# Performance work log

Measured on AMD Instinct MI355X. Metric: run time of the kernel, lower is better.

The kernel has to match this reference:

```python
import jax, jax.numpy as jnp
import numpy as np

B, T, C = 1, 2048, 1024
H = 16
D = C // H
FF = 4 * C


def layernorm(x, g, b, eps=1e-5):
    mu = jnp.mean(x, axis=-1, keepdims=True)
    var = jnp.var(x, axis=-1, keepdims=True)
    return (x - mu) * jax.lax.rsqrt(var + eps) * g + b


def setup_inputs() -> dict:
    key = jax.random.key(0)
    ks = jax.random.split(key, 16)
    s = 0.02
    return {
        "x": jax.random.normal(ks[0], (B, T, C), jnp.float32),
        "qkv_w": jax.random.normal(ks[1], (C, 3 * C), jnp.float32) * s,
        "qkv_b": jnp.zeros((3 * C,), jnp.float32),
        "out_w": jax.random.normal(ks[2], (C, C), jnp.float32) * s,
        "out_b": jnp.zeros((C,), jnp.float32),
        "ln1_g": jnp.ones((C,), jnp.float32),
        "ln1_b": jnp.zeros((C,), jnp.float32),
        "ln2_g": jnp.ones((C,), jnp.float32),
        "ln2_b": jnp.zeros((C,), jnp.float32),
        "w1": jax.random.normal(ks[3], (C, FF), jnp.float32) * s,
        "b1": jnp.zeros((FF,), jnp.float32),
        "w2": jax.random.normal(ks[4], (FF, C), jnp.float32) * s,
        "b2": jnp.zeros((C,), jnp.float32),
    }


def linear_attention(h, qkv_w, qkv_b, out_w, out_b):
    qkv = h @ qkv_w + qkv_b                      # (B,T,3C)
    q, k, v = jnp.split(qkv, 3, axis=-1)
    # (B,T,C) -> (B,H,T,D)
    reshape = lambda a: a.reshape(B, T, H, D).transpose(0, 2, 1, 3)
    q, k, v = reshape(q), reshape(k), reshape(v)
    Q = jax.nn.elu(q) + 1.0
    K = jax.nn.elu(k) + 1.0
    # causal linear attention via cumulative outer-products
    KV = jnp.einsum('bhtd,bhte->bhtde', K, v)    # (B,H,T,D,D)
    KV_cum = jnp.cumsum(KV, axis=2)
    K_cum = jnp.cumsum(K, axis=2)
    num = jnp.einsum('bhtd,bhtde->bhte', Q, KV_cum)
    den = jnp.einsum('bhtd,bhtd->bht', Q, K_cum)[..., None]
    o = num / (den + 1e-6)                       # (B,H,T,D)
    o = o.transpose(0, 2, 1, 3).reshape(B, T, C)
    return o @ out_w + out_b


def reference(x, qkv_w, qkv_b, out_w, out_b, ln1_g, ln1_b, ln2_g, ln2_b, w1, b1, w2, b2):
    x = x + linear_attention(layernorm(x, ln1_g, ln1_b), qkv_w, qkv_b, out_w, out_b)
    h = layernorm(x, ln2_g, ln2_b)
    mlp = jax.nn.gelu(h @ w1 + b1, approximate=False) @ w2 + b2
    return x + mlp
```

## Files before the change

kernel.cpp:

```cpp
#include <hip/hip_runtime.h>

typedef unsigned short u16;
typedef __bf16 bf16x8 __attribute__((ext_vector_type(8)));
typedef float f32x4 __attribute__((ext_vector_type(4)));
typedef unsigned short u16x8 __attribute__((ext_vector_type(8)));
typedef unsigned short u16x4 __attribute__((ext_vector_type(4)));

__device__ __forceinline__ float bf2f(u16 u){
  union { unsigned i; float f; } v; v.i = ((unsigned)u) << 16; return v.f;
}
__device__ __forceinline__ u16 f2bf(float f){
  union { float f; unsigned i; } v; v.f = f;
  unsigned r = v.i + 0x7FFFu + ((v.i >> 16) & 1u);
  return (u16)(r >> 16);
}
__device__ __forceinline__ float elup(float x){ return x > 0.f ? x + 1.f : expf(x); }

__device__ __forceinline__ void gload_lds16(const void* gsrc, void* ldst){
  __builtin_amdgcn_global_load_lds(
      (__attribute__((address_space(1))) void*)(unsigned long long)gsrc,
      (__attribute__((address_space(3))) void*)(unsigned)(unsigned long long)ldst,
      16, 0, 0);
}

struct TD { const float* in; u16* out; int R, Cc, cx, ntiles; };

__global__ __launch_bounds__(256) void prep(TD d0, TD d1, TD d2, TD d3,
                                            const float* __restrict__ x, const float* __restrict__ g,
                                            const float* __restrict__ b, u16* __restrict__ y){
  __shared__ u16 tile[32][33];
  __shared__ float ls[4], ls2[4];
  int bidx = blockIdx.x, tid = threadIdx.x;
  if (bidx >= 12288){
    int row = bidx - 12288;
    size_t base = (size_t)row*1024 + tid*4;
    f32x4 xv = *(const f32x4*)(x + base);
    float v0=xv[0], v1=xv[1], v2=xv[2], v3=xv[3];
    float s  = v0+v1+v2+v3;
    float s2 = v0*v0+v1*v1+v2*v2+v3*v3;
    #pragma unroll
    for (int off=32; off>0; off>>=1){ s += __shfl_xor(s, off); s2 += __shfl_xor(s2, off); }
    if ((tid & 63) == 0){ ls[tid>>6] = s; ls2[tid>>6] = s2; }
    __syncthreads();
    float ts = ls[0]+ls[1]+ls[2]+ls[3];
    float ts2 = ls2[0]+ls2[1]+ls2[2]+ls2[3];
    float mean = ts*(1.f/1024.f);
    float var  = ts2*(1.f/1024.f) - mean*mean;
    float rstd = rsqrtf(var + 1e-5f);
    f32x4 gv = *(const f32x4*)(g + tid*4);
    f32x4 bv = *(const f32x4*)(b + tid*4);
    u16x4 ov;
    ov[0]=f2bf((v0-mean)*rstd*gv[0]+bv[0]);
    ov[1]=f2bf((v1-mean)*rstd*gv[1]+bv[1]);
    ov[2]=f2bf((v2-mean)*rstd*gv[2]+bv[2]);
    ov[3]=f2bf((v3-mean)*rstd*gv[3]+bv[3]);
    *(u16x4*)(y + base) = ov;
    return;
  }
  int bb = bidx;
  TD d;
  if (bb < d0.ntiles) d = d0;
  else { bb -= d0.ntiles;
    if (bb < d1.ntiles) d = d1;
    else { bb -= d1.ntiles;
      if (bb < d2.ntiles) d = d2;
      else { bb -= d2.ntiles; d = d3; } } }
  int c0 = (bb % d.cx) * 32, r0 = (bb / d.cx) * 32;
  int tx = tid & 31, ty = tid >> 5;
  #pragma unroll
  for (int i=0;i<4;i++)
    tile[ty + i*8][tx] = f2bf(d.in[(size_t)(r0 + ty + i*8)*d.Cc + c0 + tx]);
  __syncthreads();
  #pragma unroll
  for (int i=0;i<4;i++)
    d.out[(size_t)(c0 + ty + i*8)*d.R + r0 + tx] = tile[tx][ty + i*8];
}

__global__ __launch_bounds__(256) void ln2_fused(const u16* __restrict__ P0, const u16* __restrict__ P1,
                                                 const u16* __restrict__ P2, const u16* __restrict__ P3,
                                                 const float* __restrict__ bias, const float* __restrict__ xres,
                                                 const float* __restrict__ g, const float* __restrict__ b,
                                                 float* __restrict__ x2, u16* __restrict__ h2){
  int row = blockIdx.x, tid = threadIdx.x;
  size_t base = (size_t)row*1024 + tid*4;
  u16x4 a0 = *(const u16x4*)(P0 + base);
  u16x4 a1 = *(const u16x4*)(P1 + base);
  u16x4 a2 = *(const u16x4*)(P2 + base);
  u16x4 a3 = *(const u16x4*)(P3 + base);
  f32x4 rv = *(const f32x4*)(xres + base);
  f32x4 bv = *(const f32x4*)(bias + tid*4);
  f32x4 v;
  #pragma unroll
  for (int j=0;j<4;j++) v[j] = (bf2f(a0[j])+bf2f(a1[j])) + (bf2f(a2[j])+bf2f(a3[j])) + bv[j] + rv[j];
  *(f32x4*)(x2 + base) = v;
  float s  = v[0]+v[1]+v[2]+v[3];
  float s2 = v[0]*v[0]+v[1]*v[1]+v[2]*v[2]+v[3]*v[3];
  #pragma unroll
  for (int off=32; off>0; off>>=1){ s += __shfl_xor(s, off); s2 += __shfl_xor(s2, off); }
  __shared__ float ls[4], ls2[4];
  if ((tid & 63) == 0){ ls[tid>>6] = s; ls2[tid>>6] = s2; }
  __syncthreads();
  float ts = ls[0]+ls[1]+ls[2]+ls[3];
  float ts2 = ls2[0]+ls2[1]+ls2[2]+ls2[3];
  float mean = ts*(1.f/1024.f);
  float var  = ts2*(1.f/1024.f) - mean*mean;
  float rstd = rsqrtf(var + 1e-5f);
  f32x4 gv = *(const f32x4*)(g + tid*4);
  f32x4 bb = *(const f32x4*)(b + tid*4);
  u16x4 ov;
  #pragma unroll
  for (int j=0;j<4;j++) ov[j] = f2bf((v[j]-mean)*rstd*gv[j]+bb[j]);
  *(u16x4*)(h2 + base) = ov;
}

template<int EPI>
__global__ __launch_bounds__(512, 4) void gemm_bt(const u16* __restrict__ A, const u16* __restrict__ BT,
                                                  const float* __restrict__ bias, const float* __restrict__ res,
                                                  void* __restrict__ out, int N, int K, size_t pstride){
  __shared__ u16 As[2][128*64];
  __shared__ u16 Bs[2][128*64];
  int tid = threadIdx.x;
  int w = tid >> 6, lane = tid & 63;

  unsigned flat = blockIdx.x + gridDim.x*(blockIdx.y + gridDim.y*blockIdx.z);
  unsigned nwg  = gridDim.x*gridDim.y*gridDim.z;
  unsigned logical = (flat & 7)*(nwg >> 3) + (flat >> 3);
  unsigned bx = logical % gridDim.x;
  unsigned rem = logical / gridDim.x;
  unsigned by = rem % gridDim.y;
  unsigned bz = rem / gridDim.y;

  int m0 = bx * 128, n0 = by * 128;
  int Kc = K / gridDim.z;
  int kbase = bz * Kc;
  int nt = Kc / 64;

  f32x4 acc[2][4] = {};

  int l3 = lane >> 3, l7 = lane & 7;
  const u16* aSrc = A  + (size_t)(m0 + w*16 + l3)*K + kbase + (l7 ^ l3)*8;
  const u16* bSrc = BT + (size_t)(n0 + w*16 + l3)*K + kbase + (l7 ^ l3)*8;
  int r0 = (w>>1)*32, c0 = (w&1)*64;
  int lrow = lane & 15, g4 = lane >> 4;
  int swz = (lrow & 7) << 4;

  {
    u16* aD = As[0] + w*16*64;
    u16* bD = Bs[0] + w*16*64;
    gload_lds16(aSrc,                aD);
    gload_lds16(aSrc + (size_t)8*K,  aD + 8*64);
    gload_lds16(bSrc,                bD);
    gload_lds16(bSrc + (size_t)8*K,  bD + 8*64);
  }
  __syncthreads();

  int cur = 0;
  for (int t = 0; t < nt; ++t){
    if (t + 1 < nt){
      int k0 = (t+1)*64;
      u16* aD = As[cur^1] + w*16*64;
      u16* bD = Bs[cur^1] + w*16*64;
      gload_lds16(aSrc + k0,               aD);
      gload_lds16(aSrc + (size_t)8*K + k0, aD + 8*64);
      gload_lds16(bSrc + k0,               bD);
      gload_lds16(bSrc + (size_t)8*K + k0, bD + 8*64);
    }
    const char* Ab = (const char*)As[cur];
    const char* Bb = (const char*)Bs[cur];
    #pragma unroll
    for (int kk=0; kk<2; kk++){
      int ko = (kk*64 + g4*16) ^ swz;
      bf16x8 af[2], bfv[4];
      #pragma unroll
      for (int mi=0;mi<2;mi++) af[mi]  = *(const bf16x8*)(Ab + (r0 + mi*16 + lrow)*128 + ko);
      #pragma unroll
      for (int ni=0;ni<4;ni++) bfv[ni] = *(const bf16x8*)(Bb + (c0 + ni*16 + lrow)*128 + ko);
      #pragma unroll
      for (int mi=0;mi<2;mi++)
        #pragma unroll
        for (int ni=0;ni<4;ni++)
          acc[mi][ni] = __builtin_amdgcn_mfma_f32_16x16x32_bf16(af[mi], bfv[ni], acc[mi][ni], 0, 0, 0);
    }
    __syncthreads();
    cur ^= 1;
  }

  int lgr = lane >> 4;
  u16* pout = (EPI == 3) ? ((u16*)out + (size_t)bz * pstride) : (u16*)out;
  #pragma unroll
  for (int mi=0;mi<2;mi++){
    #pragma unroll
    for (int j=0;j<4;j++){
      int row = m0 + r0 + mi*16 + lgr*4 + j;
      #pragma unroll
      for (int ni=0;ni<4;ni++){
        int col = n0 + c0 + ni*16 + lrow;
        size_t idx = (size_t)row*N + col;
        if constexpr (EPI == 3){
          pout[idx] = f2bf(acc[mi][ni][j]);
        } else {
          float v = acc[mi][ni][j] + bias[col];
          if constexpr (EPI == 0){
            ((u16*)out)[idx] = f2bf(v);
          } else {
            v = 0.5f * v * (1.f + erff(v * 0.70710678118654752f));
            ((u16*)out)[idx] = f2bf(v);
          }
        }
      }
    }
  }
}

__global__ __launch_bounds__(256) void reduce4(const u16* __restrict__ P0, const u16* __restrict__ P1,
                                               const u16* __restrict__ P2, const u16* __restrict__ P3,
                                               const float* __restrict__ bias, const float* __restrict__ res,
                                               float* __restrict__ out){
  size_t i = ((size_t)blockIdx.x*256 + threadIdx.x)*4;
  u16x4 a = *(const u16x4*)(P0 + i);
  u16x4 b = *(const u16x4*)(P1 + i);
  u16x4 c = *(const u16x4*)(P2 + i);
  u16x4 d = *(const u16x4*)(P3 + i);
  f32x4 rv = *(const f32x4*)(res + i);
  f32x4 bv = *(const f32x4*)(bias + (i & 1023));
  f32x4 o;
  #pragma unroll
  for (int j=0;j<4;j++) o[j] = (bf2f(a[j]) + bf2f(b[j])) + (bf2f(c[j]) + bf2f(d[j])) + bv[j] + rv[j];
  *(f32x4*)(out + i) = o;
}

__global__ __launch_bounds__(256) void attn_chunksum(const u16* __restrict__ qkv, float* __restrict__ S,
                                                     float* __restrict__ Ks){
  __shared__ u16 KT[64*72];
  __shared__ u16 VT[64*72];
  int c = blockIdx.x, h = blockIdx.y, tid = threadIdx.x;
  int t = tid >> 2, seg = tid & 3, e0 = seg*16;
  size_t rowb = (size_t)(c*64 + t)*3072 + h*64 + e0;
  u16x8 k0 = *(const u16x8*)(qkv + rowb + 1024);
  u16x8 k1 = *(const u16x8*)(qkv + rowb + 1032);
  u16x8 v0 = *(const u16x8*)(qkv + rowb + 2048);
  u16x8 v1 = *(const u16x8*)(qkv + rowb + 2056);
  #pragma unroll
  for (int i=0;i<8;i++){
    KT[(e0 + i)*72 + t]     = f2bf(elup(bf2f(k0[i])));
    KT[(e0 + 8 + i)*72 + t] = f2bf(elup(bf2f(k1[i])));
    VT[(e0 + i)*72 + t]     = v0[i];
    VT[(e0 + 8 + i)*72 + t] = v1[i];
  }
  __syncthreads();

  int w = tid >> 6, lane = tid & 63;
  int lr = lane & 15, lk = (lane>>4)*8, g = lane >> 4, cl = lane & 15;
  bf16x8 av_[2];
  #pragma unroll
  for (int kk=0;kk<2;kk++) av_[kk] = *(const bf16x8*)(VT + (w*16 + lr)*72 + kk*32 + lk);
  f32x4 acc[4] = {};
  #pragma unroll
  for (int di=0;di<4;di++){
    #pragma unroll
    for (int kk=0;kk<2;kk++){
      bf16x8 bk = *(const bf16x8*)(KT + (di*16 + lr)*72 + kk*32 + lk);
      acc[di] = __builtin_amdgcn_mfma_f32_16x16x32_bf16(av_[kk], bk, acc[di], 0, 0, 0);
    }
  }
  size_t base = (size_t)(h*32 + c)*4096;
  #pragma unroll
  for (int di=0;di<4;di++)
    #pragma unroll
    for (int j=0;j<4;j++)
      S[base + (size_t)(w*16 + g*4 + j)*64 + di*16 + cl] = acc[di][j];

  float s = 0.f;
  #pragma unroll
  for (int i=0;i<16;i++) s += bf2f(KT[t*72 + e0 + i]);
  s += __shfl_xor(s, 1); s += __shfl_xor(s, 2);
  if (seg == 0) Ks[(size_t)(h*32 + c)*64 + t] = s;
}

__global__ __launch_bounds__(256) void attn_prefix(float* __restrict__ S, float* __restrict__ Ks){
  int g = blockIdx.x, h = blockIdx.y, tid = threadIdx.x;
  size_t hb = (size_t)h * 32 * 4096;
  int idx = g*256 + tid;
  float run = 0.f;
  for (int c=0; c<32; c++){
    size_t p = hb + (size_t)c*4096 + idx;
    float v = S[p]; S[p] = run; run += v;
  }
  if (g == 0 && tid < 64){
    float r2 = 0.f;
    for (int c=0; c<32; c++){
      size_t p = (size_t)(h*32 + c)*64 + tid;
      float v = Ks[p]; Ks[p] = r2; r2 += v;
    }
  }
}

__global__ __launch_bounds__(256) void attn_out(const u16* __restrict__ qkv, const float* __restrict__ S,
                                                const float* __restrict__ Ks, u16* __restrict__ o){
  __shared__ u16 Qs [64*72];
  __shared__ u16 Ksh[64*72];
  __shared__ u16 VT [64*72];
  __shared__ u16 SpT[64*72];
  __shared__ u16 Am [64*72];
  __shared__ float kp[64], den[64];
  int c = blockIdx.x, h = blockIdx.y, tid = threadIdx.x;
  int t = tid >> 2, seg = tid & 3, e0 = seg*16;

  size_t rowb = (size_t)(c*64 + t)*3072 + h*64 + e0;
  u16x8 q0 = *(const u16x8*)(qkv + rowb);
  u16x8 q1 = *(const u16x8*)(qkv + rowb + 8);
  u16x8 k0 = *(const u16x8*)(qkv + rowb + 1024);
  u16x8 k1 = *(const u16x8*)(qkv + rowb + 1032);
  u16x8 v0 = *(const u16x8*)(qkv + rowb + 2048);
  u16x8 v1 = *(const u16x8*)(qkv + rowb + 2056);
  #pragma unroll
  for (int i=0;i<8;i++){
    Qs [t*72 + e0 + i]     = f2bf(elup(bf2f(q0[i])));
    Qs [t*72 + e0 + 8 + i] = f2bf(elup(bf2f(q1[i])));
    Ksh[t*72 + e0 + i]     = f2bf(elup(bf2f(k0[i])));
    Ksh[t*72 + e0 + 8 + i] = f2bf(elup(bf2f(k1[i])));
    VT [(e0 + i)*72 + t]     = v0[i];
    VT [(e0 + 8 + i)*72 + t] = v1[i];
  }
  size_t sbase = (size_t)(h*32 + c)*4096;
  {
    const f32x4* sp = (const f32x4*)(S + sbase + (size_t)t*64 + e0);
    #pragma unroll
    for (int qd=0;qd<4;qd++){
      f32x4 v = sp[qd];
      #pragma unroll
      for (int j=0;j<4;j++) SpT[t*72 + e0 + qd*4 + j] = f2bf(v[j]);
    }
  }
  if (tid < 64) kp[tid] = Ks[(size_t)(h*32 + c)*64 + tid];
  __syncthreads();

  int w = tid >> 6, lane = tid & 63;
  int lr = lane & 15, lk = (lane>>4)*8, g = lane >> 4, cl = lane & 15;

  bf16x8 aq[2];
  #pragma unroll
  for (int kk=0;kk<2;kk++) aq[kk] = *(const bf16x8*)(Qs + (w*16 + lr)*72 + kk*32 + lk);

  f32x4 acc[4] = {};
  #pragma unroll
  for (int ni=0;ni<4;ni++){
    #pragma unroll
    for (int kk=0;kk<2;kk++){
      bf16x8 bs = *(const bf16x8*)(SpT + (ni*16 + lr)*72 + kk*32 + lk);
      acc[ni] = __builtin_amdgcn_mfma_f32_16x16x32_bf16(aq[kk], bs, acc[ni], 0, 0, 0);
    }
  }
  #pragma unroll
  for (int si=0;si<4;si++){
    f32x4 qk = {};
    #pragma unroll
    for (int kk=0;kk<2;kk++){
      bf16x8 bk = *(const bf16x8*)(Ksh + (si*16 + lr)*72 + kk*32 + lk);
      qk = __builtin_amdgcn_mfma_f32_16x16x32_bf16(aq[kk], bk, qk, 0, 0, 0);
    }
    #pragma unroll
    for (int j=0;j<4;j++){
      int rowt = w*16 + g*4 + j;
      int scol = si*16 + cl;
      Am[rowt*72 + scol] = f2bf((scol <= rowt) ? qk[j] : 0.f);
    }
  }
  __syncthreads();

  {
    float dsum = 0.f;
    #pragma unroll
    for (int i=0;i<16;i++) dsum += bf2f(Am[t*72 + e0 + i]);
    #pragma unroll
    for (int i=0;i<16;i++) dsum += bf2f(Qs[t*72 + e0 + i]) * kp[e0 + i];
    dsum += __shfl_xor(dsum, 1); dsum += __shfl_xor(dsum, 2);
    if (seg == 0) den[t] = dsum;
  }
  {
    bf16x8 aa[2];
    #pragma unroll
    for (int kk=0;kk<2;kk++) aa[kk] = *(const bf16x8*)(Am + (w*16 + lr)*72 + kk*32 + lk);
    #pragma unroll
    for (int ni=0;ni<4;ni++){
      #pragma unroll
      for (int kk=0;kk<2;kk++){
        bf16x8 bv = *(const bf16x8*)(VT + (ni*16 + lr)*72 + kk*32 + lk);
        acc[ni] = __builtin_amdgcn_mfma_f32_16x16x32_bf16(aa[kk], bv, acc[ni], 0, 0, 0);
      }
    }
  }
  __syncthreads();

  #pragma unroll
  for (int j=0;j<4;j++){
    int rowt = w*16 + g*4 + j;
    float inv = 1.f/(den[rowt] + 1e-6f);
    #pragma unroll
    for (int ni=0;ni<4;ni++)
      o[(size_t)(c*64 + rowt)*1024 + h*64 + ni*16 + cl] = f2bf(acc[ni][j]*inv);
  }
}

extern "C" void kernel_launch(void* const* d_in, const int* in_sizes, int n_in,
                              void* d_out, int out_size, void* d_ws, size_t ws_size,
                              hipStream_t stream) {
  (void)in_sizes; (void)n_in; (void)out_size; (void)ws_size;
  const float* x     = (const float*)d_in[0];
  const float* qkv_w = (const float*)d_in[1];
  const float* qkv_b = (const float*)d_in[2];
  const float* out_w = (const float*)d_in[3];
  const float* out_b = (const float*)d_in[4];
  const float* ln1_g = (const float*)d_in[5];
  const float* ln1_b = (const float*)d_in[6];
  const float* ln2_g = (const float*)d_in[7];
  const float* ln2_b = (const float*)d_in[8];
  const float* w1    = (const float*)d_in[9];
  const float* b1    = (const float*)d_in[10];
  const float* w2    = (const float*)d_in[11];
  const float* b2    = (const float*)d_in[12];

  char* ws = (char*)d_ws;
  u16*   wT_qkv = (u16*)  (ws);
  u16*   wT_out = (u16*)  (ws +  6291456);
  u16*   wT_w1  = (u16*)  (ws +  8388608);
  u16*   wT_w2  = (u16*)  (ws + 16777216);
  u16*   h1     = (u16*)  (ws + 25165824);
  u16*   qkv    = (u16*)  (ws + 29360128);
  float* Ssum   = (float*)(ws + 41943040);
  float* ksum   = (float*)(ws + 50331648);
  float* x2     = (float*)(ws + 50462720);
  u16*   h2     = (u16*)  (ws + 58851328);
  u16*   o      = h1;
  u16*   a1     = qkv;
  u16*   Pa0    = (u16*)(ws + 29360128);
  size_t PaStride = 2097152;
  u16*   Pm0    = (u16*)(ws);
  u16*   Pm1    = (u16*)(ws +  4194304);
  u16*   Pm2    = (u16*)(ws +  8388608);
  u16*   Pm3    = (u16*)(ws + 12582912);
  size_t PmStride = 2097152;
  float* outp   = (float*)d_out;

  TD t0{qkv_w, wT_qkv, 1024, 3072,  96, 3072};
  TD t1{out_w, wT_out, 1024, 1024,  32, 1024};
  TD t2{w1,    wT_w1,  1024, 4096, 128, 4096};
  TD t3{w2,    wT_w2,  4096, 1024,  32, 4096};
  prep<<<14336, 256, 0, stream>>>(t0, t1, t2, t3, x, ln1_g, ln1_b, h1);

  gemm_bt<0><<<dim3(16, 24, 1), 512, 0, stream>>>(h1, wT_qkv, qkv_b, nullptr, qkv, 3072, 1024, 0);

  attn_chunksum<<<dim3(32, 16), 256, 0, stream>>>(qkv, Ssum, ksum);
  attn_prefix  <<<dim3(16, 16), 256, 0, stream>>>(Ssum, ksum);
  attn_out     <<<dim3(32, 16), 256, 0, stream>>>(qkv, Ssum, ksum, o);

  gemm_bt<3><<<dim3(16, 8, 4), 512, 0, stream>>>(o, wT_out, nullptr, nullptr, Pa0, 1024, 1024, PaStride);
  ln2_fused<<<2048, 256, 0, stream>>>(Pa0, Pa0 + PaStride, Pa0 + 2*PaStride, Pa0 + 3*PaStride,
                                      out_b, x, ln2_g, ln2_b, x2, h2);

  gemm_bt<1><<<dim3(16, 32, 1), 512, 0, stream>>>(h2, wT_w1, b1, nullptr, a1, 4096, 1024, 0);

  gemm_bt<3><<<dim3(16, 8, 4), 512, 0, stream>>>(a1, wT_w2, nullptr, nullptr, Pm0, 1024, 4096, PmStride);
  reduce4<<<2048, 256, 0, stream>>>(Pm0, Pm1, Pm2, Pm3, b2, x2, outp);
}
```

Before: 130.2 us.

## Split-K the QKV GEMM and fold partial-sum reduction into attention loads

The QKV projection now runs as a two-way split-K GEMM that writes bf16 partials. The attention chunksum and output kernels read both partials and add the bias while they load, so no separate reduction pass is needed. This is meant to put more workgroups on the GPU during the QKV GEMM. In exchange it doubles the global reads in the attention kernels and adds an extra bf16 rounding step. Separately, the weight-transpose prep kernel moves from 32x32 to 64x64 tiles so it launches fewer blocks and each thread does more work.

```diff
diff --git a/kernel.cpp b/kernel.cpp
--- a/kernel.cpp
+++ b/kernel.cpp
@@ -28,11 +28,11 @@
 __global__ __launch_bounds__(256) void prep(TD d0, TD d1, TD d2, TD d3,
                                             const float* __restrict__ x, const float* __restrict__ g,
                                             const float* __restrict__ b, u16* __restrict__ y){
-  __shared__ u16 tile[32][33];
+  __shared__ u16 tile[64][65];
   __shared__ float ls[4], ls2[4];
   int bidx = blockIdx.x, tid = threadIdx.x;
-  if (bidx >= 12288){
-    int row = bidx - 12288;
+  if (bidx >= 3072){
+    int row = bidx - 3072;
     size_t base = (size_t)row*1024 + tid*4;
     f32x4 xv = *(const f32x4*)(x + base);
     float v0=xv[0], v1=xv[1], v2=xv[2], v3=xv[3];
@@ -65,15 +65,15 @@
     else { bb -= d1.ntiles;
       if (bb < d2.ntiles) d = d2;
       else { bb -= d2.ntiles; d = d3; } } }
-  int c0 = (bb % d.cx) * 32, r0 = (bb / d.cx) * 32;
-  int tx = tid & 31, ty = tid >> 5;
-  #pragma unroll
-  for (int i=0;i<4;i++)
-    tile[ty + i*8][tx] = f2bf(d.in[(size_t)(r0 + ty + i*8)*d.Cc + c0 + tx]);
-  __syncthreads();
-  #pragma unroll
-  for (int i=0;i<4;i++)
-    d.out[(size_t)(c0 + ty + i*8)*d.R + r0 + tx] = tile[tx][ty + i*8];
+  int c0 = (bb % d.cx) * 64, r0 = (bb / d.cx) * 64;
+  int tx = tid & 63, ty = tid >> 6;
+  #pragma unroll
+  for (int i=0;i<16;i++)
+    tile[tx][ty + i*4] = f2bf(d.in[(size_t)(r0 + ty + i*4)*d.Cc + c0 + tx]);
+  __syncthreads();
+  #pragma unroll
+  for (int i=0;i<16;i++)
+    d.out[(size_t)(c0 + ty + i*4)*d.R + r0 + tx] = tile[ty + i*4][tx];
 }
 
 __global__ __launch_bounds__(256) void ln2_fused(const u16* __restrict__ P0, const u16* __restrict__ P1,
@@ -229,23 +229,29 @@
   *(f32x4*)(out + i) = o;
 }
 
-__global__ __launch_bounds__(256) void attn_chunksum(const u16* __restrict__ qkv, float* __restrict__ S,
-                                                     float* __restrict__ Ks){
+__global__ __launch_bounds__(256) void attn_chunksum(const u16* __restrict__ Q0, const u16* __restrict__ Q1,
+                                                     const float* __restrict__ qb,
+                                                     float* __restrict__ S, float* __restrict__ Ks){
   __shared__ u16 KT[64*72];
   __shared__ u16 VT[64*72];
   int c = blockIdx.x, h = blockIdx.y, tid = threadIdx.x;
   int t = tid >> 2, seg = tid & 3, e0 = seg*16;
   size_t rowb = (size_t)(c*64 + t)*3072 + h*64 + e0;
-  u16x8 k0 = *(const u16x8*)(qkv + rowb + 1024);
-  u16x8 k1 = *(const u16x8*)(qkv + rowb + 1032);
-  u16x8 v0 = *(const u16x8*)(qkv + rowb + 2048);
-  u16x8 v1 = *(const u16x8*)(qkv + rowb + 2056);
+  u16x8 k0a = *(const u16x8*)(Q0 + rowb + 1024);
+  u16x8 k1a = *(const u16x8*)(Q0 + rowb + 1032);
+  u16x8 v0a = *(const u16x8*)(Q0 + rowb + 2048);
+  u16x8 v1a = *(const u16x8*)(Q0 + rowb + 2056);
+  u16x8 k0b = *(const u16x8*)(Q1 + rowb + 1024);
+  u16x8 k1b = *(const u16x8*)(Q1 + rowb + 1032);
+  u16x8 v0b = *(const u16x8*)(Q1 + rowb + 2048);
+  u16x8 v1b = *(const u16x8*)(Q1 + rowb + 2056);
+  int cb = h*64 + e0;
   #pragma unroll
   for (int i=0;i<8;i++){
-    KT[(e0 + i)*72 + t]     = f2bf(elup(bf2f(k0[i])));
-    KT[(e0 + 8 + i)*72 + t] = f2bf(elup(bf2f(k1[i])));
-    VT[(e0 + i)*72 + t]     = v0[i];
-    VT[(e0 + 8 + i)*72 + t] = v1[i];
+    KT[(e0 + i)*72 + t]     = f2bf(elup(bf2f(k0a[i]) + bf2f(k0b[i]) + qb[1024 + cb + i]));
+    KT[(e0 + 8 + i)*72 + t] = f2bf(elup(bf2f(k1a[i]) + bf2f(k1b[i]) + qb[1024 + cb + 8 + i]));
+    VT[(e0 + i)*72 + t]     = f2bf(bf2f(v0a[i]) + bf2f(v0b[i]) + qb[2048 + cb + i]);
+    VT[(e0 + 8 + i)*72 + t] = f2bf(bf2f(v1a[i]) + bf2f(v1b[i]) + qb[2048 + cb + 8 + i]);
   }
   __syncthreads();
 
@@ -295,8 +301,10 @@
   }
 }
 
-__global__ __launch_bounds__(256) void attn_out(const u16* __restrict__ qkv, const float* __restrict__ S,
-                                                const float* __restrict__ Ks, u16* __restrict__ o){
+__global__ __launch_bounds__(256) void attn_out(const u16* __restrict__ Q0, const u16* __restrict__ Q1,
+                                                const float* __restrict__ qb,
+                                                const float* __restrict__ S, const float* __restrict__ Ks,
+                                                u16* __restrict__ o){
   __shared__ u16 Qs [64*72];
   __shared__ u16 Ksh[64*72];
   __shared__ u16 VT [64*72];
@@ -307,20 +315,27 @@
   int t = tid >> 2, seg = tid & 3, e0 = seg*16;
 
   size_t rowb = (size_t)(c*64 + t)*3072 + h*64 + e0;
-  u16x8 q0 = *(const u16x8*)(qkv + rowb);
-  u16x8 q1 = *(const u16x8*)(qkv + rowb + 8);
-  u16x8 k0 = *(const u16x8*)(qkv + rowb + 1024);
-  u16x8 k1 = *(const u16x8*)(qkv + rowb + 1032);
-  u16x8 v0 = *(const u16x8*)(qkv + rowb + 2048);
-  u16x8 v1 = *(const u16x8*)(qkv + rowb + 2056);
+  u16x8 q0a = *(const u16x8*)(Q0 + rowb);
+  u16x8 q1a = *(const u16x8*)(Q0 + rowb + 8);
+  u16x8 k0a = *(const u16x8*)(Q0 + rowb + 1024);
+  u16x8 k1a = *(const u16x8*)(Q0 + rowb + 1032);
+  u16x8 v0a = *(const u16x8*)(Q0 + rowb + 2048);
+  u16x8 v1a = *(const u16x8*)(Q0 + rowb + 2056);
+  u16x8 q0b = *(const u16x8*)(Q1 + rowb);
+  u16x8 q1b = *(const u16x8*)(Q1 + rowb + 8);
+  u16x8 k0b = *(const u16x8*)(Q1 + rowb + 1024);
+  u16x8 k1b = *(const u16x8*)(Q1 + rowb + 1032);
+  u16x8 v0b = *(const u16x8*)(Q1 + rowb + 2048);
+  u16x8 v1b = *(const u16x8*)(Q1 + rowb + 2056);
+  int cb = h*64 + e0;
   #pragma unroll
   for (int i=0;i<8;i++){
-    Qs [t*72 + e0 + i]     = f2bf(elup(bf2f(q0[i])));
-    Qs [t*72 + e0 + 8 + i] = f2bf(elup(bf2f(q1[i])));
-    Ksh[t*72 + e0 + i]     = f2bf(elup(bf2f(k0[i])));
-    Ksh[t*72 + e0 + 8 + i] = f2bf(elup(bf2f(k1[i])));
-    VT [(e0 + i)*72 + t]     = v0[i];
-    VT [(e0 + 8 + i)*72 + t] = v1[i];
+    Qs [t*72 + e0 + i]     = f2bf(elup(bf2f(q0a[i]) + bf2f(q0b[i]) + qb[cb + i]));
+    Qs [t*72 + e0 + 8 + i] = f2bf(elup(bf2f(q1a[i]) + bf2f(q1b[i]) + qb[cb + 8 + i]));
+    Ksh[t*72 + e0 + i]     = f2bf(elup(bf2f(k0a[i]) + bf2f(k0b[i]) + qb[1024 + cb + i]));
+    Ksh[t*72 + e0 + 8 + i] = f2bf(elup(bf2f(k1a[i]) + bf2f(k1b[i]) + qb[1024 + cb + 8 + i]));
+    VT [(e0 + i)*72 + t]     = f2bf(bf2f(v0a[i]) + bf2f(v0b[i]) + qb[2048 + cb + i]);
+    VT [(e0 + 8 + i)*72 + t] = f2bf(bf2f(v1a[i]) + bf2f(v1b[i]) + qb[2048 + cb + 8 + i]);
   }
   size_t sbase = (size_t)(h*32 + c)*4096;
   {
@@ -426,13 +441,15 @@
   u16*   wT_w1  = (u16*)  (ws +  8388608);
   u16*   wT_w2  = (u16*)  (ws + 16777216);
   u16*   h1     = (u16*)  (ws + 25165824);
-  u16*   qkv    = (u16*)  (ws + 29360128);
+  u16*   P0q    = (u16*)  (ws + 29360128);
   float* Ssum   = (float*)(ws + 41943040);
   float* ksum   = (float*)(ws + 50331648);
+  u16*   P1q    = (u16*)  (ws + 50462720);
+  size_t PqStride = 10551296;
   float* x2     = (float*)(ws + 50462720);
   u16*   h2     = (u16*)  (ws + 58851328);
   u16*   o      = h1;
-  u16*   a1     = qkv;
+  u16*   a1     = P0q;
   u16*   Pa0    = (u16*)(ws + 29360128);
   size_t PaStride = 2097152;
   u16*   Pm0    = (u16*)(ws);
@@ -442,17 +459,17 @@
   size_t PmStride = 2097152;
   float* outp   = (float*)d_out;
 
-  TD t0{qkv_w, wT_qkv, 1024, 3072,  96, 3072};
-  TD t1{out_w, wT_out, 1024, 1024,  32, 1024};
-  TD t2{w1,    wT_w1,  1024, 4096, 128, 4096};
-  TD t3{w2,    wT_w2,  4096, 1024,  32, 4096};
-  prep<<<14336, 256, 0, stream>>>(t0, t1, t2, t3, x, ln1_g, ln1_b, h1);
-
-  gemm_bt<0><<<dim3(16, 24, 1), 512, 0, stream>>>(h1, wT_qkv, qkv_b, nullptr, qkv, 3072, 1024, 0);
-
-  attn_chunksum<<<dim3(32, 16), 256, 0, stream>>>(qkv, Ssum, ksum);
+  TD t0{qkv_w, wT_qkv, 1024, 3072,  48,  768};
+  TD t1{out_w, wT_out, 1024, 1024,  16,  256};
+  TD t2{w1,    wT_w1,  1024, 4096,  64, 1024};
+  TD t3{w2,    wT_w2,  4096, 1024,  16, 1024};
+  prep<<<5120, 256, 0, stream>>>(t0, t1, t2, t3, x, ln1_g, ln1_b, h1);
+
+  gemm_bt<3><<<dim3(16, 24, 2), 512, 0, stream>>>(h1, wT_qkv, nullptr, nullptr, P0q, 3072, 1024, PqStride);
+
+  attn_chunksum<<<dim3(32, 16), 256, 0, stream>>>(P0q, P1q, qkv_b, Ssum, ksum);
   attn_prefix  <<<dim3(16, 16), 256, 0, stream>>>(Ssum, ksum);
-  attn_out     <<<dim3(32, 16), 256, 0, stream>>>(qkv, Ssum, ksum, o);
+  attn_out     <<<dim3(32, 16), 256, 0, stream>>>(P0q, P1q, qkv_b, Ssum, ksum, o);
 
   gemm_bt<3><<<dim3(16, 8, 4), 512, 0, stream>>>(o, wT_out, nullptr, nullptr, Pa0, 1024, 1024, PaStride);
   ln2_fused<<<2048, 256, 0, stream>>>(Pa0, Pa0 + PaStride, Pa0 + 2*PaStride, Pa0 + 3*PaStride,
```

After: 132.2 us. Within noise of the previous version (+1.6%).

## Enlarge weight-transpose tiles and move later-weight transposes into the attention chunk-sum launch

Applied to the files above, without the earlier changes.

Weight transpose tiles grow from 32x32 to 64x64, with 16 rows per thread, so far fewer blocks are launched. Only the QKV weight transpose stays in the first prep kernel beside LayerNorm1. The out-proj, W1 and W2 transposes are added as extra blocks to the attn_chunksum launch, which runs only 512 blocks of attention work. The aim is to fill an under-occupied kernel and shorten the critical path before the QKV GEMM, at the cost of a heavier, mixed-role attention launch and more shared-memory reuse.

```diff
diff --git a/kernel.cpp b/kernel.cpp
--- a/kernel.cpp
+++ b/kernel.cpp
@@ -25,14 +25,26 @@
 
 struct TD { const float* in; u16* out; int R, Cc, cx, ntiles; };
 
-__global__ __launch_bounds__(256) void prep(TD d0, TD d1, TD d2, TD d3,
-                                            const float* __restrict__ x, const float* __restrict__ g,
-                                            const float* __restrict__ b, u16* __restrict__ y){
-  __shared__ u16 tile[32][33];
+__device__ __forceinline__ void transpose_tile(const TD& d, int bb, int tid, u16 (*tile)[65]){
+  int c0 = (bb % d.cx) * 64, r0 = (bb / d.cx) * 64;
+  int tx = tid & 63, ty = tid >> 6;
+  #pragma unroll
+  for (int i=0;i<16;i++)
+    tile[tx][ty + i*4] = f2bf(d.in[(size_t)(r0 + ty + i*4)*d.Cc + c0 + tx]);
+  __syncthreads();
+  #pragma unroll
+  for (int i=0;i<16;i++)
+    d.out[(size_t)(c0 + ty + i*4)*d.R + r0 + tx] = tile[ty + i*4][tx];
+}
+
+__global__ __launch_bounds__(256) void prep1(TD t0,
+                                             const float* __restrict__ x, const float* __restrict__ g,
+                                             const float* __restrict__ b, u16* __restrict__ y){
+  __shared__ u16 tile[64][65];
   __shared__ float ls[4], ls2[4];
   int bidx = blockIdx.x, tid = threadIdx.x;
-  if (bidx >= 12288){
-    int row = bidx - 12288;
+  if (bidx >= 768){
+    int row = bidx - 768;
     size_t base = (size_t)row*1024 + tid*4;
     f32x4 xv = *(const f32x4*)(x + base);
     float v0=xv[0], v1=xv[1], v2=xv[2], v3=xv[3];
@@ -57,23 +69,7 @@
     *(u16x4*)(y + base) = ov;
     return;
   }
-  int bb = bidx;
-  TD d;
-  if (bb < d0.ntiles) d = d0;
-  else { bb -= d0.ntiles;
-    if (bb < d1.ntiles) d = d1;
-    else { bb -= d1.ntiles;
-      if (bb < d2.ntiles) d = d2;
-      else { bb -= d2.ntiles; d = d3; } } }
-  int c0 = (bb % d.cx) * 32, r0 = (bb / d.cx) * 32;
-  int tx = tid & 31, ty = tid >> 5;
-  #pragma unroll
-  for (int i=0;i<4;i++)
-    tile[ty + i*8][tx] = f2bf(d.in[(size_t)(r0 + ty + i*8)*d.Cc + c0 + tx]);
-  __syncthreads();
-  #pragma unroll
-  for (int i=0;i<4;i++)
-    d.out[(size_t)(c0 + ty + i*8)*d.R + r0 + tx] = tile[tx][ty + i*8];
+  transpose_tile(t0, bidx, tid, tile);
 }
 
 __global__ __launch_bounds__(256) void ln2_fused(const u16* __restrict__ P0, const u16* __restrict__ P1,
@@ -229,11 +225,23 @@
   *(f32x4*)(out + i) = o;
 }
 
-__global__ __launch_bounds__(256) void attn_chunksum(const u16* __restrict__ qkv, float* __restrict__ S,
-                                                     float* __restrict__ Ks){
+__global__ __launch_bounds__(256) void attn_chunksum(TD d1, TD d2, TD d3,
+                                                     const u16* __restrict__ qkv,
+                                                     float* __restrict__ S, float* __restrict__ Ks){
   __shared__ u16 KT[64*72];
   __shared__ u16 VT[64*72];
-  int c = blockIdx.x, h = blockIdx.y, tid = threadIdx.x;
+  int bidx = blockIdx.x, tid = threadIdx.x;
+  if (bidx >= 512){
+    int bb = bidx - 512;
+    TD d;
+    if (bb < d1.ntiles) d = d1;
+    else { bb -= d1.ntiles;
+      if (bb < d2.ntiles) d = d2;
+      else { bb -= d2.ntiles; d = d3; } }
+    transpose_tile(d, bb, tid, (u16(*)[65])KT);
+    return;
+  }
+  int c = bidx & 31, h = bidx >> 5;
   int t = tid >> 2, seg = tid & 3, e0 = seg*16;
   size_t rowb = (size_t)(c*64 + t)*3072 + h*64 + e0;
   u16x8 k0 = *(const u16x8*)(qkv + rowb + 1024);
@@ -442,15 +450,16 @@
   size_t PmStride = 2097152;
   float* outp   = (float*)d_out;
 
-  TD t0{qkv_w, wT_qkv, 1024, 3072,  96, 3072};
-  TD t1{out_w, wT_out, 1024, 1024,  32, 1024};
-  TD t2{w1,    wT_w1,  1024, 4096, 128, 4096};
-  TD t3{w2,    wT_w2,  4096, 1024,  32, 4096};
-  prep<<<14336, 256, 0, stream>>>(t0, t1, t2, t3, x, ln1_g, ln1_b, h1);
+  TD t0{qkv_w, wT_qkv, 1024, 3072,  48,  768};
+  TD t1{out_w, wT_out, 1024, 1024,  16,  256};
+  TD t2{w1,    wT_w1,  1024, 4096,  64, 1024};
+  TD t3{w2,    wT_w2,  4096, 1024,  16, 1024};
+
+  prep1<<<2816, 256, 0, stream>>>(t0, x, ln1_g, ln1_b, h1);
 
   gemm_bt<0><<<dim3(16, 24, 1), 512, 0, stream>>>(h1, wT_qkv, qkv_b, nullptr, qkv, 3072, 1024, 0);
 
-  attn_chunksum<<<dim3(32, 16), 256, 0, stream>>>(qkv, Ssum, ksum);
+  attn_chunksum<<<2816, 256, 0, stream>>>(t1, t2, t3, qkv, Ssum, ksum);
   attn_prefix  <<<dim3(16, 16), 256, 0, stream>>>(Ssum, ksum);
   attn_out     <<<dim3(32, 16), 256, 0, stream>>>(qkv, Ssum, ksum, o);
 
```

After: 130.0 us. No clear change (-0.1%).
